# Kernel tuning notes

Measured on AMD Instinct MI355X. Metric: run time of the kernel, lower is better.

## Reference

```python
import jax, jax.numpy as jnp
import numpy as np

CODEBOOK_SIZE = 32768
EMBED_DIM = 4


def setup_inputs() -> dict:
    key = jax.random.key(0)
    k1, k2 = jax.random.split(key)
    # [batch, temporal, channels, height, width]
    hidden_state = jax.random.normal(k1, (1, 4, EMBED_DIM, 48, 48), dtype=jnp.float32)
    # nn.Embedding weight, init uniform(-1/cb, 1/cb) as in the torch module
    embedding = jax.random.uniform(
        k2, (CODEBOOK_SIZE, EMBED_DIM), dtype=jnp.float32,
        minval=-1.0 / CODEBOOK_SIZE, maxval=1.0 / CODEBOOK_SIZE,
    )
    return {"hidden_state": hidden_state, "embedding": embedding}


def reference(hidden_state, embedding):
    b, t, c, h, w = hidden_state.shape
    # permute channels last, flatten to [N, C]
    x = jnp.transpose(hidden_state, (0, 1, 3, 4, 2)).reshape(-1, c)
    distances = (
        jnp.sum(x * x, axis=1, keepdims=True)
        + jnp.sum(embedding * embedding, axis=1)
        - 2.0 * jnp.einsum("nd,kd->nk", x, embedding)
    )
    min_encoding_indices = jnp.argmin(distances, axis=1)
    return min_encoding_indices.reshape(b, t, h, w)
```

## Files before the change

kernel.cpp:

```cpp
#include <hip/hip_runtime.h>
#include <cfloat>


#define ROWS   12
#define TILE   2048
#define BLOCK  256
#define NK     32768

__global__ __launch_bounds__(BLOCK, 3)
void vq_argmin_kernel(const float* __restrict__ hs,
                      const float4* __restrict__ cb,
                      int* __restrict__ out)
{
    __shared__ float4 sE[TILE];
    __shared__ float  sE2[TILE];
    __shared__ float  sRD[4 * ROWS];
    __shared__ int    sRI[4 * ROWS];

    const int tid = threadIdx.x;
    const int rowbase = blockIdx.x * ROWS;

    float xr0[ROWS], xr1[ROWS], xr2[ROWS], xr3[ROWS];
    float x2[ROWS];
    float best[ROWS];
    int   bidx[ROWS];

    #pragma unroll
    for (int r = 0; r < ROWS; ++r) {
        int n = rowbase + r;
        int t = n / 2304;
        int rem = n - t * 2304;
        const float* p = hs + t * 9216 + rem;
        float a0 = p[0], a1 = p[2304], a2 = p[4608], a3 = p[6912];
        xr0[r] = a0; xr1[r] = a1; xr2[r] = a2; xr3[r] = a3;
        x2[r] = __fadd_rn(__fadd_rn(__fadd_rn(__fmul_rn(a0, a0),
                                              __fmul_rn(a1, a1)),
                                    __fmul_rn(a2, a2)),
                          __fmul_rn(a3, a3));
        best[r] = FLT_MAX;
        bidx[r] = 0;
    }

    for (int tb = 0; tb < NK; tb += TILE) {
        #pragma unroll
        for (int i = 0; i < TILE / BLOCK; ++i) {
            int j = tid + i * BLOCK;
            float4 e = cb[tb + j];
            sE[j] = e;
            sE2[j] = __fadd_rn(__fadd_rn(__fadd_rn(__fmul_rn(e.x, e.x),
                                                   __fmul_rn(e.y, e.y)),
                                         __fmul_rn(e.z, e.z)),
                               __fmul_rn(e.w, e.w));
        }
        __syncthreads();

        #pragma unroll 2
        for (int i = 0; i < TILE / BLOCK; ++i) {
            int j = tid + i * BLOCK;
            float4 e = sE[j];
            float e2v = sE2[j];
            int kk = tb + j;
            #pragma unroll
            for (int r = 0; r < ROWS; ++r) {
                float dot = __builtin_fmaf(xr3[r], e.w,
                            __builtin_fmaf(xr2[r], e.z,
                            __builtin_fmaf(xr1[r], e.y,
                            __fmul_rn(xr0[r], e.x))));
                float t1 = __fadd_rn(x2[r], e2v);
                float d  = __builtin_fmaf(dot, -2.0f, t1);
                if (d < best[r]) { best[r] = d; bidx[r] = kk; }
            }
        }
        __syncthreads();
    }

    #pragma unroll
    for (int r = 0; r < ROWS; ++r) {
        float d = best[r]; int i = bidx[r];
        #pragma unroll
        for (int off = 32; off >= 1; off >>= 1) {
            float d2 = __shfl_xor(d, off, 64);
            int   i2 = __shfl_xor(i, off, 64);
            if (d2 < d || (d2 == d && i2 < i)) { d = d2; i = i2; }
        }
        best[r] = d; bidx[r] = i;
    }

    int wave = tid >> 6;
    if ((tid & 63) == 0) {
        #pragma unroll
        for (int r = 0; r < ROWS; ++r) {
            sRD[wave * ROWS + r] = best[r];
            sRI[wave * ROWS + r] = bidx[r];
        }
    }
    __syncthreads();

    if (tid < ROWS) {
        float d = sRD[tid]; int i = sRI[tid];
        #pragma unroll
        for (int w = 1; w < 4; ++w) {
            float d2 = sRD[w * ROWS + tid];
            int   i2 = sRI[w * ROWS + tid];
            if (d2 < d || (d2 == d && i2 < i)) { d = d2; i = i2; }
        }
        out[rowbase + tid] = i;
    }
}

extern "C" void kernel_launch(void* const* d_in, const int* in_sizes, int n_in,
                              void* d_out, int out_size, void* d_ws, size_t ws_size,
                              hipStream_t stream)
{
    const float*  hs = (const float*)d_in[0];
    const float4* cb = (const float4*)d_in[1];
    int* out = (int*)d_out;

    const int nrows = 9216;
    dim3 grid(nrows / ROWS), block(BLOCK);
    vq_argmin_kernel<<<grid, block, 0, stream>>>(hs, cb, out);
}
```

Measured before the change: 135.9 us.

## Double-buffer codebook tiles with async global-to-LDS loads and retune rows per block

Codebook staging now goes through `__builtin_amdgcn_global_load_lds` into two ping-pong LDS buffers, so loading the next tile overlaps with computing distances on the current one. The shared ||e||^2 array is dropped; each thread recomputes the norm of the entries it reads. Rows per block go from 12 to 9, tile size is halved, and launch bounds now target 4 blocks per SM for higher occupancy. The cost is more blocks, each streaming the full codebook, so there are more total LDS reads per output row. It also depends on the barrier draining the async LDS writes before the buffers are read.

Measured after the change: 133.4 us. Within noise of the previous version (-1.8%).

```diff
diff --git a/kernel.cpp b/kernel.cpp
--- a/kernel.cpp
+++ b/kernel.cpp
@@ -1,19 +1,58 @@
 #include <hip/hip_runtime.h>
 #include <cfloat>
+#include <stdint.h>
 
 
-#define ROWS   12
-#define TILE   2048
+#define ROWS   9
+#define TILE   1024
 #define BLOCK  256
 #define NK     32768
+#define NTILE  (NK / TILE)
+#define EPT    (TILE / BLOCK)
 
-__global__ __launch_bounds__(BLOCK, 3)
+typedef const __attribute__((address_space(1))) void GAS;
+typedef __attribute__((address_space(3))) void LAS;
+
+#define STAGE_TILE(BUF, TB)                                                   \
+    {                                                                         \
+        _Pragma("unroll")                                                     \
+        for (int c = 0; c < EPT; ++c) {                                       \
+            int slot = c * BLOCK + tid;                                       \
+            __builtin_amdgcn_global_load_lds((GAS*)(cb + (TB) + slot),        \
+                                             (LAS*)(&BUF[slot]), 16, 0, 0);   \
+        }                                                                     \
+    }
+
+#define COMPUTE_TILE(BUF, KBASE)                                              \
+    {                                                                         \
+        _Pragma("unroll")                                                     \
+        for (int i = 0; i < EPT; ++i) {                                       \
+            float4 e = BUF[tid + i * BLOCK];                                  \
+            float e2v = __fadd_rn(__fadd_rn(__fadd_rn(__fmul_rn(e.x, e.x),    \
+                                                      __fmul_rn(e.y, e.y)),   \
+                                            __fmul_rn(e.z, e.z)),             \
+                                  __fmul_rn(e.w, e.w));                       \
+            int kk = (KBASE) + tid + i * BLOCK;                               \
+            _Pragma("unroll")                                                 \
+            for (int r = 0; r < ROWS; ++r) {                                  \
+                float dot = __builtin_fmaf(xr3[r], e.w,                       \
+                            __builtin_fmaf(xr2[r], e.z,                       \
+                            __builtin_fmaf(xr1[r], e.y,                       \
+                            __fmul_rn(xr0[r], e.x))));                        \
+                float t1 = __fadd_rn(x2[r], e2v);                             \
+                float d  = __builtin_fmaf(dot, -2.0f, t1);                    \
+                if (d < best[r]) { best[r] = d; bidx[r] = kk; }               \
+            }                                                                 \
+        }                                                                     \
+    }
+
+__global__ __launch_bounds__(BLOCK, 4)
 void vq_argmin_kernel(const float* __restrict__ hs,
                       const float4* __restrict__ cb,
                       int* __restrict__ out)
 {
-    __shared__ float4 sE[TILE];
-    __shared__ float  sE2[TILE];
+    __shared__ float4 sE0[TILE];
+    __shared__ float4 sE1[TILE];
     __shared__ float  sRD[4 * ROWS];
     __shared__ int    sRI[4 * ROWS];
 
@@ -41,37 +80,15 @@
         bidx[r] = 0;
     }
 
-    for (int tb = 0; tb < NK; tb += TILE) {
-        #pragma unroll
-        for (int i = 0; i < TILE / BLOCK; ++i) {
-            int j = tid + i * BLOCK;
-            float4 e = cb[tb + j];
-            sE[j] = e;
-            sE2[j] = __fadd_rn(__fadd_rn(__fadd_rn(__fmul_rn(e.x, e.x),
-                                                   __fmul_rn(e.y, e.y)),
-                                         __fmul_rn(e.z, e.z)),
-                               __fmul_rn(e.w, e.w));
-        }
+    STAGE_TILE(sE0, 0);
+
+    for (int t = 0; t < NTILE; t += 2) {
         __syncthreads();
-
-        #pragma unroll 2
-        for (int i = 0; i < TILE / BLOCK; ++i) {
-            int j = tid + i * BLOCK;
-            float4 e = sE[j];
-            float e2v = sE2[j];
-            int kk = tb + j;
-            #pragma unroll
-            for (int r = 0; r < ROWS; ++r) {
-                float dot = __builtin_fmaf(xr3[r], e.w,
-                            __builtin_fmaf(xr2[r], e.z,
-                            __builtin_fmaf(xr1[r], e.y,
-                            __fmul_rn(xr0[r], e.x))));
-                float t1 = __fadd_rn(x2[r], e2v);
-                float d  = __builtin_fmaf(dot, -2.0f, t1);
-                if (d < best[r]) { best[r] = d; bidx[r] = kk; }
-            }
-        }
+        STAGE_TILE(sE1, (t + 1) * TILE);
+        COMPUTE_TILE(sE0, t * TILE);
         __syncthreads();
+        if (t + 2 < NTILE) STAGE_TILE(sE0, (t + 2) * TILE);
+        COMPUTE_TILE(sE1, (t + 1) * TILE);
     }
 
     #pragma unroll
```

## Stream codebook from global memory via register double-buffering instead of LDS tiles

Applied to the files above, without the earlier changes.

Removes the shared-memory codebook tile and block-wide barriers. Each thread now loads its own codebook entries straight from global memory into registers, prefetching the next chunk while it computes on the current one, and recomputes ||e||^2 inline. Rows per block drop from 12 to 9 (1024 blocks instead of 768) and the launch bound occupancy hint rises to 4. The trade-off is redundant ||e||^2 computation and codebook rereads through L2 by every block, in exchange for no LDS traffic or barriers.

Result: faster. 126.8 us (-6.7%).

```diff
diff --git a/kernel.cpp b/kernel.cpp
--- a/kernel.cpp
+++ b/kernel.cpp
@@ -2,20 +2,19 @@
 #include <cfloat>
 
 
-#define ROWS   12
-#define TILE   2048
+#define ROWS   9
 #define BLOCK  256
 #define NK     32768
+#define EPT    4
+#define CHUNK  (BLOCK * EPT)
 
-__global__ __launch_bounds__(BLOCK, 3)
+__global__ __launch_bounds__(BLOCK, 4)
 void vq_argmin_kernel(const float* __restrict__ hs,
                       const float4* __restrict__ cb,
                       int* __restrict__ out)
 {
-    __shared__ float4 sE[TILE];
-    __shared__ float  sE2[TILE];
-    __shared__ float  sRD[4 * ROWS];
-    __shared__ int    sRI[4 * ROWS];
+    __shared__ float sRD[4 * ROWS];
+    __shared__ int   sRI[4 * ROWS];
 
     const int tid = threadIdx.x;
     const int rowbase = blockIdx.x * ROWS;
@@ -41,25 +40,23 @@
         bidx[r] = 0;
     }
 
-    for (int tb = 0; tb < NK; tb += TILE) {
+    float4 ce[EPT], ne[EPT];
+    #pragma unroll
+    for (int j = 0; j < EPT; ++j) ce[j] = cb[tid + j * BLOCK];
+
+    for (int tb = 0; tb < NK; tb += CHUNK) {
+        int nb = tb + CHUNK < NK ? tb + CHUNK : tb;
         #pragma unroll
-        for (int i = 0; i < TILE / BLOCK; ++i) {
-            int j = tid + i * BLOCK;
-            float4 e = cb[tb + j];
-            sE[j] = e;
-            sE2[j] = __fadd_rn(__fadd_rn(__fadd_rn(__fmul_rn(e.x, e.x),
-                                                   __fmul_rn(e.y, e.y)),
-                                         __fmul_rn(e.z, e.z)),
-                               __fmul_rn(e.w, e.w));
-        }
-        __syncthreads();
+        for (int j = 0; j < EPT; ++j) ne[j] = cb[nb + tid + j * BLOCK];
 
-        #pragma unroll 2
-        for (int i = 0; i < TILE / BLOCK; ++i) {
-            int j = tid + i * BLOCK;
-            float4 e = sE[j];
-            float e2v = sE2[j];
-            int kk = tb + j;
+        #pragma unroll
+        for (int j = 0; j < EPT; ++j) {
+            float4 e = ce[j];
+            float e2v = __fadd_rn(__fadd_rn(__fadd_rn(__fmul_rn(e.x, e.x),
+                                                      __fmul_rn(e.y, e.y)),
+                                            __fmul_rn(e.z, e.z)),
+                                  __fmul_rn(e.w, e.w));
+            int kk = tb + tid + j * BLOCK;
             #pragma unroll
             for (int r = 0; r < ROWS; ++r) {
                 float dot = __builtin_fmaf(xr3[r], e.w,
@@ -71,7 +68,9 @@
                 if (d < best[r]) { best[r] = d; bidx[r] = kk; }
             }
         }
-        __syncthreads();
+
+        #pragma unroll
+        for (int j = 0; j < EPT; ++j) ce[j] = ne[j];
     }
 
     #pragma unroll
```
